# Kernel tuning notes

Measured on AMD Instinct MI355X. Metric: run time of the kernel, lower is better.

## Reference

```python
import jax, jax.numpy as jnp
import numpy as np

N_NODES = 100000
N_EDGES = 3200000
IN_CH = 13
HID = 64
DIMS = [(IN_CH, HID), (HID, HID), (HID, HID), (HID, 1)]


def setup_inputs() -> dict:
    key = jax.random.key(0)
    ks = jax.random.split(key, 2 + 3 * len(DIMS))
    inp = {
        "x": jax.random.normal(ks[0], (N_NODES, IN_CH), dtype=jnp.float32),
        "edge_index": jax.random.randint(ks[1], (2, N_EDGES), 0, N_NODES, dtype=jnp.int64),
    }
    for l, (din, dout) in enumerate(DIMS):
        s = 1.0 / np.sqrt(din)
        inp[f"Wl{l}"] = jax.random.uniform(ks[2 + 3 * l], (din, dout), jnp.float32, -s, s)
        inp[f"bl{l}"] = jax.random.uniform(ks[3 + 3 * l], (dout,), jnp.float32, -s, s)
        inp[f"Wr{l}"] = jax.random.uniform(ks[4 + 3 * l], (din, dout), jnp.float32, -s, s)
    return inp


def _sage_forward(x, edge_index, params):
    src, dst = edge_index[0], edge_index[1]
    # in-degree for mean aggregation (constant across layers)
    deg = jax.ops.segment_sum(jnp.ones((edge_index.shape[1],), x.dtype), dst,
                              num_segments=N_NODES)
    inv_deg = (1.0 / jnp.maximum(deg, 1.0))[:, None]  # [N,1]
    n_layers = len(params)
    for i, (Wl, bl, Wr) in enumerate(params):
        msg = x[src]  # [E, d] neighbor gather
        mean_neigh = jax.ops.segment_sum(msg, dst, num_segments=N_NODES) * inv_deg
        x = mean_neigh @ Wl + bl + x @ Wr  # lin_l(aggr) + lin_r(root)
        if i != n_layers - 1:
            x = jax.nn.relu(x)
    return x.reshape(-1)  # [N]


def reference(x, edge_index, Wl0, bl0, Wr0, Wl1, bl1, Wr1, Wl2, bl2, Wr2, Wl3, bl3, Wr3):
    params = [(Wl0, bl0, Wr0), (Wl1, bl1, Wr1), (Wl2, bl2, Wr2), (Wl3, bl3, Wr3)]
    return _sage_forward(x, edge_index, params)
```

## Files before the change

### kernel.cpp

```cpp
#include <hip/hip_runtime.h>
#include <hip/hip_fp16.h>

#define NT 256
#define NPB 256
#define MAXBUK 512
#define A3_TILE 4096
#define NSTRIP 16
#define STRIP_SH 13
#define CAP 12288

typedef _Float16 half8 __attribute__((ext_vector_type(8)));
typedef float floatx4 __attribute__((ext_vector_type(4)));


__global__ void init_bcur(int* __restrict__ bcur, int nbuk) {
    int b = blockIdx.x * blockDim.x + threadIdx.x;
    if (b < nbuk) bcur[b] = b * CAP;
}

__global__ __launch_bounds__(256) void partition(const int* __restrict__ ei, int E,
                                                 int* __restrict__ bcur,
                                                 unsigned int* __restrict__ pairs) {
    __shared__ int h[MAXBUK];
    __shared__ int base[MAXBUK];
    int t = threadIdx.x;
    for (int i = t; i < MAXBUK; i += 256) h[i] = 0;
    __syncthreads();
    int e0 = blockIdx.x * A3_TILE + t * 16;
    int src[16], dst[16];
    if (((E & 3) == 0) && (e0 + 15 < E)) {
        const int4* p4s = (const int4*)(ei + e0);
        const int4* p4d = (const int4*)(ei + E + e0);
#pragma unroll
        for (int j4 = 0; j4 < 4; j4++) {
            int4 s4 = p4s[j4];
            int4 d4 = p4d[j4];
            src[j4 * 4 + 0] = s4.x; dst[j4 * 4 + 0] = d4.x;
            src[j4 * 4 + 1] = s4.y; dst[j4 * 4 + 1] = d4.y;
            src[j4 * 4 + 2] = s4.z; dst[j4 * 4 + 2] = d4.z;
            src[j4 * 4 + 3] = s4.w; dst[j4 * 4 + 3] = d4.w;
        }
    } else {
#pragma unroll
        for (int j = 0; j < 16; j++) {
            int e = e0 + j;
            if (e < E) {
                src[j] = ei[e];
                dst[j] = ei[E + e];
            } else {
                dst[j] = -1;
            }
        }
    }
#pragma unroll
    for (int j = 0; j < 16; j++)
        if (dst[j] >= 0) atomicAdd(&h[dst[j] >> 8], 1);
    __syncthreads();
    for (int b = t; b < MAXBUK; b += 256) {
        int c = h[b];
        base[b] = c ? atomicAdd(&bcur[b], c) : 0;
        h[b] = 0;
    }
    __syncthreads();
#pragma unroll
    for (int j = 0; j < 16; j++) {
        if (dst[j] >= 0) {
            int bkt = dst[j] >> 8;
            int r = atomicAdd(&h[bkt], 1);
            pairs[base[bkt] + r] = ((unsigned)(dst[j] & (NPB - 1)) << 24) | (unsigned)src[j];
        }
    }
}

__global__ __launch_bounds__(512) void build_bucket(const unsigned int* __restrict__ pairs,
                                                    const int* __restrict__ bcur,
                                                    int* __restrict__ csr_off,
                                                    int* __restrict__ csr_end,
                                                    int* __restrict__ csr_src,
                                                    float* __restrict__ invd, int N) {
    __shared__ int h2[NPB * NSTRIP];
    __shared__ int tsum[512];
    int b = blockIdx.x, t = threadIdx.x;
    int gb0 = b * CAP;
    int cnt = bcur[b] - gb0;
    int gb1 = gb0 + cnt;
    int nb0 = b << 8;
    int nn = min(NPB, N - nb0);
    for (int i = t; i < NPB * NSTRIP; i += 512) h2[i] = 0;
    __syncthreads();
    for (int i = gb0 + t; i < gb1; i += 512) {
        unsigned p = pairs[i];
        int ld = p >> 24;
        int st = (int)((p & 0xFFFFFFu) >> STRIP_SH);
        atomicAdd(&h2[ld * NSTRIP + st], 1);
    }
    __syncthreads();
    if (t < nn) {
        int d = 0;
#pragma unroll
        for (int ss = 0; ss < NSTRIP; ss++) d += h2[t * NSTRIP + ss];
        invd[nb0 + t] = 1.0f / (float)max(d, 1);
    }
    int v[8];
    int loc = 0;
#pragma unroll
    for (int j = 0; j < 8; j++) {
        v[j] = h2[t * 8 + j];
        loc += v[j];
    }
    tsum[t] = loc;
    __syncthreads();
    for (int off = 1; off < 512; off <<= 1) {
        int xv = 0;
        if (t >= off) xv = tsum[t - off];
        __syncthreads();
        tsum[t] += xv;
        __syncthreads();
    }
    int run = (t == 0) ? 0 : tsum[t - 1];
#pragma unroll
    for (int j = 0; j < 8; j++) {
        h2[t * 8 + j] = run;
        run += v[j];
    }
    __syncthreads();
    if (t < nn) {
        csr_off[nb0 + t] = gb0 + h2[t * NSTRIP];
        int endv = (t == NPB - 1) ? cnt : h2[(t + 1) * NSTRIP];
        csr_end[nb0 + t] = gb0 + endv;
    }
    __syncthreads();
    for (int i = gb0 + t; i < gb1; i += 512) {
        unsigned p = pairs[i];
        int ld = p >> 24;
        unsigned srcv = p & 0xFFFFFFu;
        int st = (int)(srcv >> STRIP_SH);
        int pos = atomicAdd(&h2[ld * NSTRIP + st], 1);
        csr_src[gb0 + pos] = (int)srcv;
    }
}


__device__ inline void acc8(float* acc, uint4 hv) {
    const __half2* hp = reinterpret_cast<const __half2*>(&hv);
#pragma unroll
    for (int j = 0; j < 4; j++) {
        float2 f = __half22float2(hp[j]);
        acc[2 * j] += f.x;
        acc[2 * j + 1] += f.y;
    }
}

__device__ inline void acc4v(float* acc, uint2 hv) {
    const __half2* hp = reinterpret_cast<const __half2*>(&hv);
#pragma unroll
    for (int j = 0; j < 2; j++) {
        float2 f = __half22float2(hp[j]);
        acc[2 * j] += f.x;
        acc[2 * j + 1] += f.y;
    }
}

__global__ void pad_x(const float* __restrict__ x, __half* __restrict__ xroot0, int N) {
    int i = blockIdx.x * blockDim.x + threadIdx.x;
    if (i < N * 16) {
        int n = i >> 4, c = i & 15;
        float v = (c < 13) ? x[n * 13 + c] : 0.f;
        xroot0[i] = __float2half(v);
    }
}

__global__ __launch_bounds__(512) void fused0(
    const __half* __restrict__ xroot0, const int* __restrict__ off, const int* __restrict__ end,
    const int* __restrict__ csr, const float* __restrict__ invd,
    const float* __restrict__ Wl, const float* __restrict__ bl, const float* __restrict__ Wr,
    __half* __restrict__ xroot1, int N) {
    __shared__ _Float16 act[64 * 40];
    __shared__ _Float16 wt[64 * 40];
    __shared__ float bs[64];
    int t = threadIdx.x;
    for (int i = t; i < 2048; i += 512) {
        int k = i >> 6, c = i & 63;
        float v;
        if (k < 16) v = (k < 13) ? Wl[k * 64 + c] : 0.f;
        else {
            int kk = k - 16;
            v = (kk < 13) ? Wr[kk * 64 + c] : 0.f;
        }
        wt[c * 40 + k] = (_Float16)v;
    }
    if (t < 64) bs[t] = bl[t];
    int n0 = blockIdx.x * 64;
    if (t < 256) {
        int node = t >> 2, cc4 = (t & 3) * 4;
        int n = min(n0 + node, N - 1);
        uint2 rv = *(const uint2*)(xroot0 + (size_t)n * 16 + cc4);
        *(uint2*)&act[node * 40 + 16 + cc4] = rv;
    }
    int lane = t & 63, wid = t >> 6;
    int g = lane >> 2, c4 = (lane & 3) * 4;
#pragma unroll 1
    for (int rr = 0; rr < 8; rr++) {
        int nloc = rr * 8 + wid;
        int n = min(n0 + nloc, N - 1);
        float sc = invd[n];
        int e0 = off[n], e1 = end[n];
        float acc[4] = {0, 0, 0, 0};
        int e = e0;
        for (; e + 31 < e1; e += 32) {
            int s0 = csr[e + g];
            int s1 = csr[e + 16 + g];
            uint2 h0 = *(const uint2*)(xroot0 + (size_t)s0 * 16 + c4);
            uint2 h1 = *(const uint2*)(xroot0 + (size_t)s1 * 16 + c4);
            acc4v(acc, h0);
            acc4v(acc, h1);
        }
        if (e + 15 < e1) {
            uint2 h0 = *(const uint2*)(xroot0 + (size_t)csr[e + g] * 16 + c4);
            acc4v(acc, h0);
            e += 16;
        }
        if (e + g < e1) {
            uint2 h0 = *(const uint2*)(xroot0 + (size_t)csr[e + g] * 16 + c4);
            acc4v(acc, h0);
        }
#pragma unroll
        for (int o = 4; o <= 32; o <<= 1) {
#pragma unroll
            for (int j = 0; j < 4; j++) acc[j] += __shfl_xor(acc[j], o);
        }
        if (lane < 4) {
            __half2 p[2];
            p[0] = __floats2half2_rn(acc[0] * sc, acc[1] * sc);
            p[1] = __floats2half2_rn(acc[2] * sc, acc[3] * sc);
            *(uint2*)&act[nloc * 40 + lane * 4] = *(const uint2*)p;
        }
    }
    __syncthreads();
    if (wid < 4) {
        int row = lane & 15, kg = lane >> 4;
        half8 a = *(const half8*)&act[(wid * 16 + row) * 40 + kg * 8];
        floatx4 ac[4];
#pragma unroll
        for (int tt = 0; tt < 4; tt++) ac[tt] = (floatx4){0.f, 0.f, 0.f, 0.f};
#pragma unroll
        for (int tt = 0; tt < 4; tt++) {
            half8 b = *(const half8*)&wt[(tt * 16 + row) * 40 + kg * 8];
            ac[tt] = __builtin_amdgcn_mfma_f32_16x16x32_f16(a, b, ac[tt], 0, 0, 0);
        }
#pragma unroll
        for (int tt = 0; tt < 4; tt++) {
            int col = tt * 16 + row;
            float bias = bs[col];
#pragma unroll
            for (int r = 0; r < 4; r++) {
                int n = n0 + wid * 16 + kg * 4 + r;
                if (n < N)
                    xroot1[(size_t)n * 64 + col] = __float2half(fmaxf(ac[tt][r] + bias, 0.f));
            }
        }
    }
}

template <int LAST>
__global__ __launch_bounds__(512) void fused_layer(
    const __half* __restrict__ xroot, const int* __restrict__ off, const int* __restrict__ end,
    const int* __restrict__ csr, const float* __restrict__ invd,
    const float* __restrict__ Wl, const float* __restrict__ bl, const float* __restrict__ Wr,
    __half* __restrict__ xnext,
    const float* __restrict__ Wl3, const float* __restrict__ bl3, const float* __restrict__ Wr3,
    float* __restrict__ s3, float* __restrict__ r3, int N) {
    __shared__ _Float16 act[64 * 136];
    __shared__ _Float16 wt[64 * 136];
    __shared__ float bs[64];
    int t = threadIdx.x;
    for (int i = t; i < 8192; i += 512) {
        int k = i >> 6, c = i & 63;
        float v = (k < 64) ? Wl[k * 64 + c] : Wr[(k - 64) * 64 + c];
        wt[c * 136 + k] = (_Float16)v;
    }
    if (t < 64) bs[t] = bl[t];
    int n0 = blockIdx.x * 64;
    {
        int node = t >> 3, cc8 = (t & 7) * 8;
        int n = min(n0 + node, N - 1);
        uint4 rv = *(const uint4*)(xroot + (size_t)n * 64 + cc8);
        *(uint4*)&act[node * 136 + 64 + cc8] = rv;
    }
    int lane = t & 63, wid = t >> 6;
    int g = lane >> 3, c8 = (lane & 7) * 8;
#pragma unroll 1
    for (int rr = 0; rr < 8; rr++) {
        int nloc = rr * 8 + wid;
        int n = min(n0 + nloc, N - 1);
        float sc = invd[n];
        int e0 = off[n], e1 = end[n];
        float acc[8] = {0, 0, 0, 0, 0, 0, 0, 0};
        int e = e0;
        for (; e + 31 < e1; e += 32) {
            int s0 = csr[e + g];
            int s1 = csr[e + 8 + g];
            int s2 = csr[e + 16 + g];
            int s3v = csr[e + 24 + g];
            uint4 h0 = *(const uint4*)(xroot + (size_t)s0 * 64 + c8);
            uint4 h1 = *(const uint4*)(xroot + (size_t)s1 * 64 + c8);
            uint4 h2 = *(const uint4*)(xroot + (size_t)s2 * 64 + c8);
            uint4 h3 = *(const uint4*)(xroot + (size_t)s3v * 64 + c8);
            acc8(acc, h0);
            acc8(acc, h1);
            acc8(acc, h2);
            acc8(acc, h3);
        }
        if (e + 15 < e1) {
            int s0 = csr[e + g];
            int s1 = csr[e + 8 + g];
            uint4 h0 = *(const uint4*)(xroot + (size_t)s0 * 64 + c8);
            uint4 h1 = *(const uint4*)(xroot + (size_t)s1 * 64 + c8);
            acc8(acc, h0);
            acc8(acc, h1);
            e += 16;
        }
        if (e + 7 < e1) {
            uint4 h0 = *(const uint4*)(xroot + (size_t)csr[e + g] * 64 + c8);
            acc8(acc, h0);
            e += 8;
        }
        if (e + g < e1) {
            uint4 h0 = *(const uint4*)(xroot + (size_t)csr[e + g] * 64 + c8);
            acc8(acc, h0);
        }
#pragma unroll
        for (int o = 8; o <= 32; o <<= 1) {
#pragma unroll
            for (int j = 0; j < 8; j++) acc[j] += __shfl_xor(acc[j], o);
        }
        if (lane < 8) {
            __half2 p[4];
#pragma unroll
            for (int j = 0; j < 4; j++)
                p[j] = __floats2half2_rn(acc[2 * j] * sc, acc[2 * j + 1] * sc);
            *(uint4*)&act[nloc * 136 + lane * 8] = *(const uint4*)p;
        }
    }
    __syncthreads();
    if (wid < 4) {
        int row = lane & 15, kg = lane >> 4;
        const _Float16* abase = &act[(wid * 16 + row) * 136 + kg * 8];
        half8 a[4];
#pragma unroll
        for (int kk = 0; kk < 4; kk++) a[kk] = *(const half8*)(abase + kk * 32);
        floatx4 ac[4];
#pragma unroll
        for (int tt = 0; tt < 4; tt++) ac[tt] = (floatx4){0.f, 0.f, 0.f, 0.f};
#pragma unroll
        for (int kk = 0; kk < 4; kk++) {
#pragma unroll
            for (int tt = 0; tt < 4; tt++) {
                half8 b = *(const half8*)&wt[(tt * 16 + row) * 136 + kk * 32 + kg * 8];
                ac[tt] = __builtin_amdgcn_mfma_f32_16x16x32_f16(a[kk], b, ac[tt], 0, 0, 0);
            }
        }
        if (LAST == 0) {
#pragma unroll
            for (int tt = 0; tt < 4; tt++) {
                int col = tt * 16 + row;
                float bias = bs[col];
#pragma unroll
                for (int r = 0; r < 4; r++) {
                    int n = n0 + wid * 16 + kg * 4 + r;
                    if (n < N)
                        xnext[(size_t)n * 64 + col] = __float2half(fmaxf(ac[tt][r] + bias, 0.f));
                }
            }
        } else {
            float wl3v[4], wr3v[4];
#pragma unroll
            for (int tt = 0; tt < 4; tt++) {
                int col = tt * 16 + row;
                wl3v[tt] = Wl3[col];
                wr3v[tt] = Wr3[col];
            }
            float b3 = bl3[0];
            float sp[4], rp[4];
#pragma unroll
            for (int r = 0; r < 4; r++) {
                float spv = 0.f, rpv = 0.f;
#pragma unroll
                for (int tt = 0; tt < 4; tt++) {
                    float v = fmaxf(ac[tt][r] + bs[tt * 16 + row], 0.f);
                    spv += v * wl3v[tt];
                    rpv += v * wr3v[tt];
                }
                sp[r] = spv;
                rp[r] = rpv;
            }
#pragma unroll
            for (int o = 1; o <= 8; o <<= 1) {
#pragma unroll
                for (int r = 0; r < 4; r++) {
                    sp[r] += __shfl_xor(sp[r], o);
                    rp[r] += __shfl_xor(rp[r], o);
                }
            }
            if (row == 0) {
#pragma unroll
                for (int r = 0; r < 4; r++) {
                    int n = n0 + wid * 16 + kg * 4 + r;
                    if (n < N) {
                        s3[n] = sp[r];
                        r3[n] = rp[r] + b3;
                    }
                }
            }
        }
    }
}

__global__ void sage_last_scalar(
    const float* __restrict__ s3, const float* __restrict__ r3, const int* __restrict__ off,
    const int* __restrict__ end, const int* __restrict__ csr, const float* __restrict__ invd,
    float* __restrict__ out, int N) {
    int n = blockIdx.x * blockDim.x + threadIdx.x;
    if (n >= N) return;
    int e0 = off[n], e1 = end[n];
    float acc = 0.f;
    int e = e0;
    for (; e + 3 < e1; e += 4) {
        float a0 = s3[csr[e]], a1 = s3[csr[e + 1]], a2 = s3[csr[e + 2]], a3 = s3[csr[e + 3]];
        acc += a0 + a1 + a2 + a3;
    }
    for (; e < e1; e++) acc += s3[csr[e]];
    out[n] = acc * invd[n] + r3[n];
}


extern "C" void kernel_launch(void* const* d_in, const int* in_sizes, int n_in,
                              void* d_out, int out_size, void* d_ws, size_t ws_size,
                              hipStream_t stream) {
    const float* x0 = (const float*)d_in[0];
    const int* ei = (const int*)d_in[1];
    const float* Wl[4] = {(const float*)d_in[2], (const float*)d_in[5], (const float*)d_in[8],
                          (const float*)d_in[11]};
    const float* bl[4] = {(const float*)d_in[3], (const float*)d_in[6], (const float*)d_in[9],
                          (const float*)d_in[12]};
    const float* Wr[4] = {(const float*)d_in[4], (const float*)d_in[7], (const float*)d_in[10],
                          (const float*)d_in[13]};
    float* out = (float*)d_out;

    const int N = in_sizes[0] / 13;
    const int E = in_sizes[1] / 2;
    const int nbuk = (N + NPB - 1) / NPB;

    char* w = (char*)d_ws;
    auto carve = [&](size_t bytes) {
        void* p = (void*)w;
        w += (bytes + 255) & ~size_t(255);
        return p;
    };
    int* bcur = (int*)carve((size_t)MAXBUK * 4);
    unsigned int* pairs = (unsigned int*)carve((size_t)nbuk * CAP * 4);
    int* csr_off = (int*)carve((size_t)N * 4);
    int* csr_end = (int*)carve((size_t)N * 4);
    int* csr_src = (int*)carve((size_t)nbuk * CAP * 4);
    float* invd = (float*)carve((size_t)N * 4);
    __half* xroot0 = (__half*)carve((size_t)N * 16 * 2);
    __half* xroot1 = (__half*)carve((size_t)N * 64 * 2);
    __half* xroot2 = (__half*)carve((size_t)N * 64 * 2);
    float* s3 = (float*)carve((size_t)N * 4);
    float* r3 = (float*)carve((size_t)N * 4);

    init_bcur<<<(nbuk + 255) / 256, 256, 0, stream>>>(bcur, nbuk);
    partition<<<(E + A3_TILE - 1) / A3_TILE, 256, 0, stream>>>(ei, E, bcur, pairs);
    build_bucket<<<nbuk, 512, 0, stream>>>(pairs, bcur, csr_off, csr_end, csr_src, invd, N);

    pad_x<<<(N * 16 + NT - 1) / NT, NT, 0, stream>>>(x0, xroot0, N);

    int gblk = (N + 63) / 64;
    fused0<<<gblk, 512, 0, stream>>>(xroot0, csr_off, csr_end, csr_src, invd,
                                     Wl[0], bl[0], Wr[0], xroot1, N);
    fused_layer<0><<<gblk, 512, 0, stream>>>(xroot1, csr_off, csr_end, csr_src, invd,
                                             Wl[1], bl[1], Wr[1], xroot2,
                                             nullptr, nullptr, nullptr, nullptr, nullptr, N);
    fused_layer<1><<<gblk, 512, 0, stream>>>(xroot2, csr_off, csr_end, csr_src, invd,
                                             Wl[2], bl[2], Wr[2], nullptr,
                                             Wl[3], bl[3], Wr[3], s3, r3, N);
    sage_last_scalar<<<(N + NT - 1) / NT, NT, 0, stream>>>(s3, r3, csr_off, csr_end, csr_src,
                                                           invd, out, N);
}
```

Before: 249.1 us.

## Store hidden features as 16-channel planes and gather plane-by-plane for cache locality

Hidden activations are stored as four planes of 16 channels each instead of interleaved 64-channel rows. The layer kernels gather one plane at a time, so each pass touches a much smaller working set that is more likely to stay resident in L2. Blocks now process 128 nodes, with 4 lanes per node walking its edge list serially, which replaces the earlier cooperative edge split across 8 lane groups. The trade-off is that each edge's index is re-read once per plane, gathers are narrower 8-byte loads, and per-node loops are longer, which may expose more latency.

```diff
diff --git a/kernel.cpp b/kernel.cpp
--- a/kernel.cpp
+++ b/kernel.cpp
@@ -141,16 +141,6 @@
 }
 
 
-__device__ inline void acc8(float* acc, uint4 hv) {
-    const __half2* hp = reinterpret_cast<const __half2*>(&hv);
-#pragma unroll
-    for (int j = 0; j < 4; j++) {
-        float2 f = __half22float2(hp[j]);
-        acc[2 * j] += f.x;
-        acc[2 * j + 1] += f.y;
-    }
-}
-
 __device__ inline void acc4v(float* acc, uint2 hv) {
     const __half2* hp = reinterpret_cast<const __half2*>(&hv);
 #pragma unroll
@@ -174,7 +164,7 @@
     const __half* __restrict__ xroot0, const int* __restrict__ off, const int* __restrict__ end,
     const int* __restrict__ csr, const float* __restrict__ invd,
     const float* __restrict__ Wl, const float* __restrict__ bl, const float* __restrict__ Wr,
-    __half* __restrict__ xroot1, int N) {
+    __half* __restrict__ xn, int N) {
     __shared__ _Float16 act[64 * 40];
     __shared__ _Float16 wt[64 * 40];
     __shared__ float bs[64];
@@ -238,6 +228,7 @@
     }
     __syncthreads();
     if (wid < 4) {
+        size_t N16 = (size_t)N * 16;
         int row = lane & 15, kg = lane >> 4;
         half8 a = *(const half8*)&act[(wid * 16 + row) * 40 + kg * 8];
         floatx4 ac[4];
@@ -250,13 +241,13 @@
         }
 #pragma unroll
         for (int tt = 0; tt < 4; tt++) {
-            int col = tt * 16 + row;
-            float bias = bs[col];
+            float bias = bs[tt * 16 + row];
 #pragma unroll
             for (int r = 0; r < 4; r++) {
                 int n = n0 + wid * 16 + kg * 4 + r;
                 if (n < N)
-                    xroot1[(size_t)n * 64 + col] = __float2half(fmaxf(ac[tt][r] + bias, 0.f));
+                    xn[(size_t)tt * N16 + (size_t)n * 16 + row] =
+                        __float2half(fmaxf(ac[tt][r] + bias, 0.f));
             }
         }
     }
@@ -264,13 +255,13 @@
 
 template <int LAST>
 __global__ __launch_bounds__(512) void fused_layer(
-    const __half* __restrict__ xroot, const int* __restrict__ off, const int* __restrict__ end,
+    const __half* __restrict__ xr, const int* __restrict__ off, const int* __restrict__ end,
     const int* __restrict__ csr, const float* __restrict__ invd,
     const float* __restrict__ Wl, const float* __restrict__ bl, const float* __restrict__ Wr,
-    __half* __restrict__ xnext,
+    __half* __restrict__ xn,
     const float* __restrict__ Wl3, const float* __restrict__ bl3, const float* __restrict__ Wr3,
     float* __restrict__ s3, float* __restrict__ r3, int N) {
-    __shared__ _Float16 act[64 * 136];
+    __shared__ _Float16 act[128 * 136];
     __shared__ _Float16 wt[64 * 136];
     __shared__ float bs[64];
     int t = threadIdx.x;
@@ -280,70 +271,51 @@
         wt[c * 136 + k] = (_Float16)v;
     }
     if (t < 64) bs[t] = bl[t];
-    int n0 = blockIdx.x * 64;
+
+    int n0 = blockIdx.x * 128;
+    int lane = t & 63, wid = t >> 6;
+    int nloc = wid * 16 + (lane >> 2);
+    int c4 = (lane & 3) * 4;
+    int n = min(n0 + nloc, N - 1);
+    int e0 = off[n], e1 = end[n];
+    float sc = invd[n];
+    size_t N16 = (size_t)N * 16;
+    int rnode = t >> 2;
+    int rn = min(n0 + rnode, N - 1);
+    int rc4 = (t & 3) * 4;
+
+#pragma unroll 1
+    for (int p = 0; p < 4; p++) {
+        const __half* plane = xr + (size_t)p * N16;
+        {
+            uint2 rv = *(const uint2*)(plane + (size_t)rn * 16 + rc4);
+            *(uint2*)&act[rnode * 136 + 64 + p * 16 + rc4] = rv;
+        }
+        float acc[4] = {0, 0, 0, 0};
+        int e = e0;
+        for (; e + 3 < e1; e += 4) {
+            int s0 = csr[e], s1 = csr[e + 1], s2 = csr[e + 2], s3v = csr[e + 3];
+            uint2 h0 = *(const uint2*)(plane + (size_t)s0 * 16 + c4);
+            uint2 h1 = *(const uint2*)(plane + (size_t)s1 * 16 + c4);
+            uint2 h2 = *(const uint2*)(plane + (size_t)s2 * 16 + c4);
+            uint2 h3 = *(const uint2*)(plane + (size_t)s3v * 16 + c4);
+            acc4v(acc, h0);
+            acc4v(acc, h1);
+            acc4v(acc, h2);
+            acc4v(acc, h3);
+        }
+        for (; e < e1; e++) {
+            uint2 h0 = *(const uint2*)(plane + (size_t)csr[e] * 16 + c4);
+            acc4v(acc, h0);
+        }
+        __half2 pk[2];
+        pk[0] = __floats2half2_rn(acc[0] * sc, acc[1] * sc);
+        pk[1] = __floats2half2_rn(acc[2] * sc, acc[3] * sc);
+        *(uint2*)&act[nloc * 136 + p * 16 + c4] = *(const uint2*)pk;
+    }
+    __syncthreads();
+
     {
-        int node = t >> 3, cc8 = (t & 7) * 8;
-        int n = min(n0 + node, N - 1);
-        uint4 rv = *(const uint4*)(xroot + (size_t)n * 64 + cc8);
-        *(uint4*)&act[node * 136 + 64 + cc8] = rv;
-    }
-    int lane = t & 63, wid = t >> 6;
-    int g = lane >> 3, c8 = (lane & 7) * 8;
-#pragma unroll 1
-    for (int rr = 0; rr < 8; rr++) {
-        int nloc = rr * 8 + wid;
-        int n = min(n0 + nloc, N - 1);
-        float sc = invd[n];
-        int e0 = off[n], e1 = end[n];
-        float acc[8] = {0, 0, 0, 0, 0, 0, 0, 0};
-        int e = e0;
-        for (; e + 31 < e1; e += 32) {
-            int s0 = csr[e + g];
-            int s1 = csr[e + 8 + g];
-            int s2 = csr[e + 16 + g];
-            int s3v = csr[e + 24 + g];
-            uint4 h0 = *(const uint4*)(xroot + (size_t)s0 * 64 + c8);
-            uint4 h1 = *(const uint4*)(xroot + (size_t)s1 * 64 + c8);
-            uint4 h2 = *(const uint4*)(xroot + (size_t)s2 * 64 + c8);
-            uint4 h3 = *(const uint4*)(xroot + (size_t)s3v * 64 + c8);
-            acc8(acc, h0);
-            acc8(acc, h1);
-            acc8(acc, h2);
-            acc8(acc, h3);
-        }
-        if (e + 15 < e1) {
-            int s0 = csr[e + g];
-            int s1 = csr[e + 8 + g];
-            uint4 h0 = *(const uint4*)(xroot + (size_t)s0 * 64 + c8);
-            uint4 h1 = *(const uint4*)(xroot + (size_t)s1 * 64 + c8);
-            acc8(acc, h0);
-            acc8(acc, h1);
-            e += 16;
-        }
-        if (e + 7 < e1) {
-            uint4 h0 = *(const uint4*)(xroot + (size_t)csr[e + g] * 64 + c8);
-            acc8(acc, h0);
-            e += 8;
-        }
-        if (e + g < e1) {
-            uint4 h0 = *(const uint4*)(xroot + (size_t)csr[e + g] * 64 + c8);
-            acc8(acc, h0);
-        }
-#pragma unroll
-        for (int o = 8; o <= 32; o <<= 1) {
-#pragma unroll
-            for (int j = 0; j < 8; j++) acc[j] += __shfl_xor(acc[j], o);
-        }
-        if (lane < 8) {
-            __half2 p[4];
-#pragma unroll
-            for (int j = 0; j < 4; j++)
-                p[j] = __floats2half2_rn(acc[2 * j] * sc, acc[2 * j + 1] * sc);
-            *(uint4*)&act[nloc * 136 + lane * 8] = *(const uint4*)p;
-        }
-    }
-    __syncthreads();
-    if (wid < 4) {
         int row = lane & 15, kg = lane >> 4;
         const _Float16* abase = &act[(wid * 16 + row) * 136 + kg * 8];
         half8 a[4];
@@ -363,13 +335,13 @@
         if (LAST == 0) {
 #pragma unroll
             for (int tt = 0; tt < 4; tt++) {
-                int col = tt * 16 + row;
-                float bias = bs[col];
+                float bias = bs[tt * 16 + row];
 #pragma unroll
                 for (int r = 0; r < 4; r++) {
-                    int n = n0 + wid * 16 + kg * 4 + r;
-                    if (n < N)
-                        xnext[(size_t)n * 64 + col] = __float2half(fmaxf(ac[tt][r] + bias, 0.f));
+                    int nw = n0 + wid * 16 + kg * 4 + r;
+                    if (nw < N)
+                        xn[(size_t)tt * N16 + (size_t)nw * 16 + row] =
+                            __float2half(fmaxf(ac[tt][r] + bias, 0.f));
                 }
             }
         } else {
@@ -405,10 +377,10 @@
             if (row == 0) {
 #pragma unroll
                 for (int r = 0; r < 4; r++) {
-                    int n = n0 + wid * 16 + kg * 4 + r;
-                    if (n < N) {
-                        s3[n] = sp[r];
-                        r3[n] = rp[r] + b3;
+                    int nw = n0 + wid * 16 + kg * 4 + r;
+                    if (nw < N) {
+                        s3[nw] = sp[r];
+                        r3[nw] = rp[r] + b3;
                     }
                 }
             }
@@ -475,9 +447,10 @@
 
     pad_x<<<(N * 16 + NT - 1) / NT, NT, 0, stream>>>(x0, xroot0, N);
 
-    int gblk = (N + 63) / 64;
-    fused0<<<gblk, 512, 0, stream>>>(xroot0, csr_off, csr_end, csr_src, invd,
-                                     Wl[0], bl[0], Wr[0], xroot1, N);
+    int gblk0 = (N + 63) / 64;
+    int gblk = (N + 127) / 128;
+    fused0<<<gblk0, 512, 0, stream>>>(xroot0, csr_off, csr_end, csr_src, invd,
+                                      Wl[0], bl[0], Wr[0], xroot1, N);
     fused_layer<0><<<gblk, 512, 0, stream>>>(xroot1, csr_off, csr_end, csr_src, invd,
                                              Wl[1], bl[1], Wr[1], xroot2,
                                              nullptr, nullptr, nullptr, nullptr, nullptr, N);
```

Measured after the change: 415.4 us. 1.67x slower.
